# Kernel optimization log

Measured on AMD Instinct MI355X. Metric: run time of the kernel, lower is better.

The kernel has to match this reference:

```python
import jax, jax.numpy as jnp
import numpy as np
from jax import lax

N, C_IN, C_OUT = 1, 16, 32
D = W = H = 48
K = 9                      # num_points (snake kernel size)
CENTER = K // 2
EXTEND_SCOPE = 1.0
EPS = 1e-5
GN_GROUPS = C_OUT // 4
DN = ('NCDHW', 'OIDHW', 'NCDHW')


def conv3d(x, w, strides, padding):
    return lax.conv_general_dilated(x, w, strides, padding, dimension_numbers=DN)


def snake_cumsum(off):
    # off: [N, K, D, W, H]. Cumulative offsets outward from the center point,
    # center forced to 0 (matches the sequential loop in _coordinate_map_3D).
    lower = jnp.flip(jnp.cumsum(jnp.flip(off[:, :CENTER], 1), 1), 1)
    upper = jnp.cumsum(off[:, CENTER + 1:], 1)
    zero = jnp.zeros_like(off[:, :1])
    return jnp.concatenate([lower, zero, upper], axis=1)


def coordinate_map_morph0(off):
    # off: [N, 6K, D, W, H]; morph==0 uses z_offset1 (chans [0,K)) and y_offset1 ([K,2K)).
    cz = snake_cumsum(off[:, :K])
    cy = snake_cumsum(off[:, K:2 * K])
    dt = off.dtype
    zb = jnp.arange(D, dtype=dt)[None, None, :, None, None]
    yb = jnp.arange(W, dtype=dt)[None, None, None, :, None]
    xb = (jnp.arange(H, dtype=dt)[None, None, None, None, :]
          + (jnp.arange(K, dtype=dt) - CENTER)[None, :, None, None, None])
    z = zb + EXTEND_SCOPE * cz                      # [N,K,D,W,H]
    y = yb + EXTEND_SCOPE * cy
    x = jnp.broadcast_to(xb, z.shape)

    def rearr(c):  # [N,K,D,W,H] -> [N,D,W,H*K]  (h-major, k-minor, as in torch permute/reshape)
        return jnp.transpose(c, (0, 2, 3, 4, 1)).reshape(c.shape[0], D, W, H * K)

    return rearr(z), rearr(y), rearr(x)


def trilinear(feat, z, y, x):
    # feat [N,C,D,W,H]; z,y,x [N,D,W,H*K] float coords -> [N,C,D,W,H*K]
    z = jnp.clip(z, 0.0, D - 1.0)
    y = jnp.clip(y, 0.0, W - 1.0)
    x = jnp.clip(x, 0.0, H - 1.0)
    z0 = jnp.clip(jnp.floor(z).astype(jnp.int32), 0, D - 1); z1 = jnp.clip(z0 + 1, 0, D - 1)
    y0 = jnp.clip(jnp.floor(y).astype(jnp.int32), 0, W - 1); y1 = jnp.clip(y0 + 1, 0, W - 1)
    x0 = jnp.clip(jnp.floor(x).astype(jnp.int32), 0, H - 1); x1 = jnp.clip(x0 + 1, 0, H - 1)
    featl = jnp.transpose(feat, (0, 2, 3, 4, 1))  # [N,D,W,H,C]
    b = jnp.arange(feat.shape[0])[:, None, None, None]
    g = lambda zi, yi, xi: featl[b, zi, yi, xi]   # [N,D,W,H*K,C]
    f = feat.dtype
    wz0 = (z1.astype(f) - z)[..., None]; wz1 = (z - z0.astype(f))[..., None]
    wy0 = (y1.astype(f) - y)[..., None]; wy1 = (y - y0.astype(f))[..., None]
    wx0 = (x1.astype(f) - x)[..., None]; wx1 = (x - x0.astype(f))[..., None]
    out = (g(z0, y0, x0) * wz0 * wy0 * wx0 + g(z0, y0, x1) * wz0 * wy0 * wx1
         + g(z0, y1, x0) * wz0 * wy1 * wx0 + g(z0, y1, x1) * wz0 * wy1 * wx1
         + g(z1, y0, x0) * wz1 * wy0 * wx0 + g(z1, y0, x1) * wz1 * wy0 * wx1
         + g(z1, y1, x0) * wz1 * wy1 * wx0 + g(z1, y1, x1) * wz1 * wy1 * wx1)
    return jnp.transpose(out, (0, 4, 1, 2, 3))


def group_norm(x, gamma, beta):
    n = x.shape[0]
    xg = x.reshape(n, GN_GROUPS, -1)
    mu = xg.mean(-1, keepdims=True)
    var = xg.var(-1, keepdims=True)
    xg = (xg - mu) * lax.rsqrt(var + EPS)
    return xg.reshape(x.shape) * gamma[None, :, None, None, None] + beta[None, :, None, None, None]


def setup_inputs() -> dict:
    key = jax.random.key(0)
    ks = jax.random.split(key, 6)
    s = 0.05
    return {
        'x': jax.random.normal(ks[0], (N, C_IN, D, W, H), jnp.float32),
        'ow': jax.random.normal(ks[1], (6 * K, C_IN, 3, 3, 3), jnp.float32) * s,
        'ob': jax.random.normal(ks[2], (6 * K,), jnp.float32) * s,
        'bn_gamma': jnp.ones((6 * K,), jnp.float32),
        'bn_beta': jnp.zeros((6 * K,), jnp.float32),
        'bn_mean': jnp.zeros((6 * K,), jnp.float32),
        'bn_var': jnp.ones((6 * K,), jnp.float32),
        'dw': jax.random.normal(ks[3], (C_OUT, C_IN, 1, 1, K), jnp.float32) * s,
        'db': jax.random.normal(ks[4], (C_OUT,), jnp.float32) * s,
        'gn_gamma': jnp.ones((C_OUT,), jnp.float32),
        'gn_beta': jnp.zeros((C_OUT,), jnp.float32),
    }


def reference(x, ow, ob, bn_gamma, bn_beta, bn_mean, bn_var, dw, db, gn_gamma, gn_beta):
    # offset branch: conv3x3x3 -> BN (eval) -> tanh
    off = conv3d(x, ow, (1, 1, 1), 'SAME') + ob[None, :, None, None, None]
    c = lambda v: v[None, :, None, None, None]
    off = (off - c(bn_mean)) * lax.rsqrt(c(bn_var) + EPS) * c(bn_gamma) + c(bn_beta)
    off = jnp.tanh(off)
    # deformed sampling coordinates (morph 0: spread along x/height axis)
    zc, yc, xc = coordinate_map_morph0(off)
    deformed = trilinear(x, zc, yc, xc)           # [N,C,D,W,H*K]
    # snake conv: kernel (1,1,K) stride (1,1,K) -> [N,C_OUT,D,W,H]
    out = conv3d(deformed, dw, (1, 1, K), 'VALID') + db[None, :, None, None, None]
    out = group_norm(out, gn_gamma, gn_beta)
    return jax.nn.relu(out)
```

## Files before the change

kernel.cpp:

```cpp
#include <hip/hip_runtime.h>

#define DD    48
#define SP    (48*48*48)
#define CIN   16
#define COUT  32
#define KK    9
#define NG    8
#define EPSV  1e-5f

__global__ __launch_bounds__(256) void k_xt(const float* __restrict__ x,
                                            float* __restrict__ xt,
                                            float* __restrict__ stats) {
    int t = threadIdx.x;
    int vb = t >> 2, c = t & 3;
    int v = blockIdx.x * 64 + vb;
    float4 o;
    o.x = x[(4 * c + 0) * SP + v];
    o.y = x[(4 * c + 1) * SP + v];
    o.z = x[(4 * c + 2) * SP + v];
    o.w = x[(4 * c + 3) * SP + v];
    *reinterpret_cast<float4*>(xt + v * 16 + 4 * c) = o;
    if (blockIdx.x == 0) stats[t] = 0.0f;
}

__global__ __launch_bounds__(256) void k_off18(
    const float* __restrict__ xt,  const float* __restrict__ ow,
    const float* __restrict__ ob,  const float* __restrict__ bng,
    const float* __restrict__ bnb, const float* __restrict__ bnm,
    const float* __restrict__ bnv, float* __restrict__ off)
{
    __shared__ float cw[27 * 4 * 72];
    __shared__ float bnsc[18], bnsh[18];

    for (int i = threadIdx.x; i < 27 * CIN * 18; i += 256) {
        int ch = i % 18; int r = i / 18; int ci = r % CIN; int tap = r / CIN;
        int c = ci >> 2, j = ci & 3;
        cw[(tap * 4 + c) * 72 + ch * 4 + j] = ow[(ch * CIN + ci) * 27 + tap];
    }
    if (threadIdx.x < 18) {
        int ch = threadIdx.x;
        float sc = bng[ch] * rsqrtf(bnv[ch] + EPSV);
        bnsc[ch] = sc;
        bnsh[ch] = (ob[ch] - bnm[ch]) * sc + bnb[ch];
    }
    __syncthreads();

    const int nwg = SP / 64;
    int bid = (int)blockIdx.x;
    bid = (bid & 7) * (nwg >> 3) + (bid >> 3);

    const int t  = threadIdx.x;
    const int c  = t & 3;
    const int vb = t >> 2;
    const int v  = bid * 64 + vb;
    const int h = v % DD, w = (v / DD) % DD, d = v / (DD * DD);

    const float* xc = xt + 4 * c;

    float a18[18];
#pragma unroll
    for (int ch = 0; ch < 18; ++ch) a18[ch] = 0.0f;

#pragma unroll
    for (int kd = 0; kd < 3; ++kd) {
        int z = d + kd - 1; bool okz = (unsigned)z < (unsigned)DD;
#pragma unroll
        for (int kw = 0; kw < 3; ++kw) {
            int yy = w + kw - 1; bool oky = (unsigned)yy < (unsigned)DD;
#pragma unroll
            for (int kh = 0; kh < 3; ++kh) {
                int xx = h + kh - 1;
                if (okz && oky && (unsigned)xx < (unsigned)DD) {
                    int tap = (kd * 3 + kw) * 3 + kh;
                    float4 xv = *reinterpret_cast<const float4*>(
                        xc + ((z * DD + yy) * DD + xx) * 16);
                    const float4* wrow = reinterpret_cast<const float4*>(
                        &cw[(tap * 4 + c) * 72]);
#pragma unroll
                    for (int ch = 0; ch < 18; ++ch) {
                        float4 w4 = wrow[ch];
                        a18[ch] += w4.x * xv.x + w4.y * xv.y
                                 + w4.z * xv.z + w4.w * xv.w;
                    }
                }
            }
        }
    }

#pragma unroll
    for (int ch = 0; ch < 18; ++ch) {
        a18[ch] += __shfl_xor(a18[ch], 1);
        a18[ch] += __shfl_xor(a18[ch], 2);
        a18[ch] = tanhf(a18[ch] * bnsc[ch] + bnsh[ch]);
    }

#pragma unroll
    for (int cc = 0; cc < 4; ++cc) {
        if (c == cc) {
#pragma unroll
            for (int j = 0; j < 4; ++j)
                off[(cc * 4 + j) * SP + v] = a18[cc * 4 + j];
        }
    }
    if (c == 0) off[16 * SP + v] = a18[16];
    if (c == 1) off[17 * SP + v] = a18[17];
}

__global__ __launch_bounds__(256) void k_snake(
    const float* __restrict__ xt,  const float* __restrict__ off,
    const float* __restrict__ dw,  const float* __restrict__ db,
    float* __restrict__ pre,       float* __restrict__ stats)
{
    __shared__ float wl[KK * 4 * 132];
    __shared__ float lstat[16];
    for (int i = threadIdx.x; i < KK * CIN * COUT; i += 256) {
        int co = i % COUT; int r = i / COUT; int ci = r % CIN; int k = r / CIN;
        int c = ci >> 2, j = ci & 3;
        wl[(k * 4 + c) * 132 + co * 4 + j] = dw[(co * CIN + ci) * KK + k];
    }
    if (threadIdx.x < 16) lstat[threadIdx.x] = 0.0f;
    __syncthreads();

    const int nwg = SP / 64;
    int bid = (int)blockIdx.x;
    bid = (bid & 7) * (nwg >> 3) + (bid >> 3);

    const int t  = threadIdx.x;
    const int c  = t & 3;
    const int vb = t >> 2;
    const int v  = bid * 64 + vb;
    const int h = v % DD, w = (v / DD) % DD, d = v / (DD * DD);

    float cz[9], cy[9];
    cz[4] = 0.0f; cy[4] = 0.0f;
    {
        float rz = 0.0f, ry = 0.0f;
#pragma unroll
        for (int k = 3; k >= 0; --k) {
            rz += off[k * SP + v];        cz[k] = rz;
            ry += off[(KK + k) * SP + v]; cy[k] = ry;
        }
    }
    {
        float rz = 0.0f, ry = 0.0f;
#pragma unroll
        for (int k = 5; k < KK; ++k) {
            rz += off[k * SP + v];        cz[k] = rz;
            ry += off[(KK + k) * SP + v]; cy[k] = ry;
        }
    }

    float w00[9], w01[9], w10[9], w11[9];
    int   b00[9], b01[9], b10[9], b11[9];
#pragma unroll
    for (int k = 0; k < 9; ++k) {
        int xcol = h + k - 4;
        float m = (xcol >= DD - 1) ? 0.0f : 1.0f;
        if (xcol < 0 || xcol >= DD - 1) xcol = 0;
        float zf = fminf(fmaxf((float)d + cz[k], 0.0f), 47.0f);
        float yf = fminf(fmaxf((float)w + cy[k], 0.0f), 47.0f);
        int z0 = (int)zf, y0 = (int)yf;
        int z1 = min(z0 + 1, 47), y1 = min(y0 + 1, 47);
        float wz1 = zf - (float)z0, wz0 = (float)z1 - zf;
        float wy1 = yf - (float)y0, wy0 = (float)y1 - yf;
        w00[k] = wz0 * wy0 * m; w01[k] = wz0 * wy1 * m;
        w10[k] = wz1 * wy0 * m; w11[k] = wz1 * wy1 * m;
        b00[k] = ((z0 * DD + y0) * DD + xcol) * 16;
        b01[k] = ((z0 * DD + y1) * DD + xcol) * 16;
        b10[k] = ((z1 * DD + y0) * DD + xcol) * 16;
        b11[k] = ((z1 * DD + y1) * DD + xcol) * 16;
    }

    const float* base = xt + 4 * c;
    float acc[COUT];
#pragma unroll
    for (int co = 0; co < COUT; ++co) acc[co] = 0.0f;

    float4 A0, A1, A2, A3, B0, B1, B2, B3;

#define LOADP(P, k)                                                        \
    (P##0) = *reinterpret_cast<const float4*>(base + b00[k]);              \
    (P##1) = *reinterpret_cast<const float4*>(base + b01[k]);              \
    (P##2) = *reinterpret_cast<const float4*>(base + b10[k]);              \
    (P##3) = *reinterpret_cast<const float4*>(base + b11[k]);

#define FMAP(P, k)                                                         \
    {                                                                      \
        float s0 = w00[k]*(P##0).x + w01[k]*(P##1).x + w10[k]*(P##2).x + w11[k]*(P##3).x; \
        float s1 = w00[k]*(P##0).y + w01[k]*(P##1).y + w10[k]*(P##2).y + w11[k]*(P##3).y; \
        float s2 = w00[k]*(P##0).z + w01[k]*(P##1).z + w10[k]*(P##2).z + w11[k]*(P##3).z; \
        float s3 = w00[k]*(P##0).w + w01[k]*(P##1).w + w10[k]*(P##2).w + w11[k]*(P##3).w; \
        const float4* wrow = reinterpret_cast<const float4*>(&wl[((k)*4 + c) * 132]); \
        _Pragma("unroll")                                                  \
        for (int co = 0; co < COUT; ++co) {                                \
            float4 w4 = wrow[co];                                          \
            acc[co] += w4.x * s0 + w4.y * s1 + w4.z * s2 + w4.w * s3;      \
        }                                                                  \
    }

    LOADP(A, 0)
    LOADP(B, 1) FMAP(A, 0)
    LOADP(A, 2) FMAP(B, 1)
    LOADP(B, 3) FMAP(A, 2)
    LOADP(A, 4) FMAP(B, 3)
    LOADP(B, 5) FMAP(A, 4)
    LOADP(A, 6) FMAP(B, 5)
    LOADP(B, 7) FMAP(A, 6)
    LOADP(A, 8) FMAP(B, 7)
    FMAP(A, 8)
#undef LOADP
#undef FMAP

#pragma unroll
    for (int co = 0; co < COUT; ++co) {
        acc[co] += __shfl_xor(acc[co], 1);
        acc[co] += __shfl_xor(acc[co], 2);
        acc[co] += db[co];
    }

#pragma unroll
    for (int cc = 0; cc < 4; ++cc) {
        if (c == cc) {
#pragma unroll
            for (int j = 0; j < 8; ++j)
                pre[(cc * 8 + j) * SP + v] = acc[cc * 8 + j];
        }
    }

#pragma unroll
    for (int g = 0; g < NG; ++g) {
        float a0 = acc[4*g], a1 = acc[4*g+1], a2 = acc[4*g+2], a3 = acc[4*g+3];
        float s  = a0 + a1 + a2 + a3;
        float ss = a0*a0 + a1*a1 + a2*a2 + a3*a3;
#pragma unroll
        for (int o = 4; o <= 32; o <<= 1) {
            s  += __shfl_xor(s,  o);
            ss += __shfl_xor(ss, o);
        }
        if ((t & 63) == 0) {
            atomicAdd(&lstat[g],      s);
            atomicAdd(&lstat[NG + g], ss);
        }
    }
    __syncthreads();
    if (t < 16) atomicAdd(&stats[t * 16], lstat[t]);
}

__global__ __launch_bounds__(256) void k_gn(
    float* __restrict__ buf, const float* __restrict__ stats,
    const float* __restrict__ gamma, const float* __restrict__ beta)
{
    int idx  = blockIdx.x * 256 + threadIdx.x;
    int base = idx * 4;
    int ch = base / SP, g = ch >> 2;

    const float inv_n = 1.0f / (4.0f * (float)SP);
    float mean = stats[g * 16] * inv_n;
    float var  = stats[(NG + g) * 16] * inv_n - mean * mean;
    float rs   = rsqrtf(var + EPSV);
    float ga   = gamma[ch] * rs;
    float be   = beta[ch] - mean * ga;

    float4 p = *reinterpret_cast<const float4*>(buf + base);
    float4 o;
    o.x = fmaxf(p.x * ga + be, 0.0f);
    o.y = fmaxf(p.y * ga + be, 0.0f);
    o.z = fmaxf(p.z * ga + be, 0.0f);
    o.w = fmaxf(p.w * ga + be, 0.0f);
    *reinterpret_cast<float4*>(buf + base) = o;
}

extern "C" void kernel_launch(void* const* d_in, const int* in_sizes, int n_in,
                              void* d_out, int out_size, void* d_ws, size_t ws_size,
                              hipStream_t stream)
{
    const float* x   = (const float*)d_in[0];
    const float* ow  = (const float*)d_in[1];
    const float* ob  = (const float*)d_in[2];
    const float* bng = (const float*)d_in[3];
    const float* bnb = (const float*)d_in[4];
    const float* bnm = (const float*)d_in[5];
    const float* bnv = (const float*)d_in[6];
    const float* dw  = (const float*)d_in[7];
    const float* db  = (const float*)d_in[8];
    const float* gng = (const float*)d_in[9];
    const float* gnb = (const float*)d_in[10];
    float* out = (float*)d_out;

    float* xt    = (float*)d_ws;
    float* stats = xt + CIN * SP;
    float* off   = stats + 256;

    k_xt   <<<SP / 64, 256, 0, stream>>>(x, xt, stats);
    k_off18<<<SP / 64, 256, 0, stream>>>(xt, ow, ob, bng, bnb, bnm, bnv, off);
    k_snake<<<SP / 64, 256, 0, stream>>>(xt, off, dw, db, out, stats);
    k_gn   <<<(COUT * SP / 4) / 256, 256, 0, stream>>>(out, stats, gng, gnb);
}
```

Measured before the change: 223.0 us.

## Compute two adjacent voxels per thread in offset conv and snake kernels

The offset convolution now gives each thread two neighbouring h positions. It loads four input columns per row and reuses them across the three kh taps, and the shared-memory weights are reused for both outputs. The snake kernel also handles two voxels per thread with 128-thread blocks. It interleaves the cumulative offset sum with the tap processing, skips fully masked taps, and uses float2 loads and stores. This roughly doubles per-thread register use and lowers thread count, which may reduce occupancy and latency hiding.

```diff
diff --git a/kernel.cpp b/kernel.cpp
--- a/kernel.cpp
+++ b/kernel.cpp
@@ -45,42 +45,53 @@
     }
     __syncthreads();
 
-    const int nwg = SP / 64;
+    const int nwg = SP / 128;
     int bid = (int)blockIdx.x;
     bid = (bid & 7) * (nwg >> 3) + (bid >> 3);
 
     const int t  = threadIdx.x;
     const int c  = t & 3;
-    const int vb = t >> 2;
-    const int v  = bid * 64 + vb;
-    const int h = v % DD, w = (v / DD) % DD, d = v / (DD * DD);
+    const int vq = t >> 2;
+    const int v0 = bid * 128 + vq * 2;
+    const int h0 = v0 % DD;
+    const int w  = (v0 / DD) % DD;
+    const int d  = v0 / (DD * DD);
 
     const float* xc = xt + 4 * c;
 
-    float a18[18];
-#pragma unroll
-    for (int ch = 0; ch < 18; ++ch) a18[ch] = 0.0f;
+    float a0[18], a1[18];
+#pragma unroll
+    for (int ch = 0; ch < 18; ++ch) { a0[ch] = 0.0f; a1[ch] = 0.0f; }
 
 #pragma unroll
     for (int kd = 0; kd < 3; ++kd) {
         int z = d + kd - 1; bool okz = (unsigned)z < (unsigned)DD;
 #pragma unroll
         for (int kw = 0; kw < 3; ++kw) {
-            int yy = w + kw - 1; bool oky = (unsigned)yy < (unsigned)DD;
-#pragma unroll
-            for (int kh = 0; kh < 3; ++kh) {
-                int xx = h + kh - 1;
-                if (okz && oky && (unsigned)xx < (unsigned)DD) {
+            int yy = w + kw - 1;
+            if (okz && (unsigned)yy < (unsigned)DD) {
+                const float* row = xc + ((z * DD + yy) * DD) * 16;
+                float4 xv[4];
+#pragma unroll
+                for (int j = 0; j < 4; ++j) {
+                    int col = h0 - 1 + j;
+                    float4 val = make_float4(0.f, 0.f, 0.f, 0.f);
+                    if ((unsigned)col < (unsigned)DD)
+                        val = *reinterpret_cast<const float4*>(row + col * 16);
+                    xv[j] = val;
+                }
+#pragma unroll
+                for (int kh = 0; kh < 3; ++kh) {
                     int tap = (kd * 3 + kw) * 3 + kh;
-                    float4 xv = *reinterpret_cast<const float4*>(
-                        xc + ((z * DD + yy) * DD + xx) * 16);
                     const float4* wrow = reinterpret_cast<const float4*>(
                         &cw[(tap * 4 + c) * 72]);
 #pragma unroll
                     for (int ch = 0; ch < 18; ++ch) {
                         float4 w4 = wrow[ch];
-                        a18[ch] += w4.x * xv.x + w4.y * xv.y
-                                 + w4.z * xv.z + w4.w * xv.w;
+                        a0[ch] += w4.x * xv[kh].x + w4.y * xv[kh].y
+                                + w4.z * xv[kh].z + w4.w * xv[kh].w;
+                        a1[ch] += w4.x * xv[kh+1].x + w4.y * xv[kh+1].y
+                                + w4.z * xv[kh+1].z + w4.w * xv[kh+1].w;
                     }
                 }
             }
@@ -89,31 +100,37 @@
 
 #pragma unroll
     for (int ch = 0; ch < 18; ++ch) {
-        a18[ch] += __shfl_xor(a18[ch], 1);
-        a18[ch] += __shfl_xor(a18[ch], 2);
-        a18[ch] = tanhf(a18[ch] * bnsc[ch] + bnsh[ch]);
+        a0[ch] += __shfl_xor(a0[ch], 1);
+        a0[ch] += __shfl_xor(a0[ch], 2);
+        a0[ch] = tanhf(a0[ch] * bnsc[ch] + bnsh[ch]);
+        a1[ch] += __shfl_xor(a1[ch], 1);
+        a1[ch] += __shfl_xor(a1[ch], 2);
+        a1[ch] = tanhf(a1[ch] * bnsc[ch] + bnsh[ch]);
     }
 
 #pragma unroll
     for (int cc = 0; cc < 4; ++cc) {
         if (c == cc) {
 #pragma unroll
-            for (int j = 0; j < 4; ++j)
-                off[(cc * 4 + j) * SP + v] = a18[cc * 4 + j];
-        }
-    }
-    if (c == 0) off[16 * SP + v] = a18[16];
-    if (c == 1) off[17 * SP + v] = a18[17];
-}
-
-__global__ __launch_bounds__(256) void k_snake(
+            for (int j = 0; j < 4; ++j) {
+                int ch = cc * 4 + j;
+                *reinterpret_cast<float2*>(&off[ch * SP + v0]) =
+                    make_float2(a0[ch], a1[ch]);
+            }
+        }
+    }
+    if (c == 0) *reinterpret_cast<float2*>(&off[16 * SP + v0]) = make_float2(a0[16], a1[16]);
+    if (c == 1) *reinterpret_cast<float2*>(&off[17 * SP + v0]) = make_float2(a0[17], a1[17]);
+}
+
+__global__ __launch_bounds__(128) void k_snake(
     const float* __restrict__ xt,  const float* __restrict__ off,
     const float* __restrict__ dw,  const float* __restrict__ db,
     float* __restrict__ pre,       float* __restrict__ stats)
 {
     __shared__ float wl[KK * 4 * 132];
     __shared__ float lstat[16];
-    for (int i = threadIdx.x; i < KK * CIN * COUT; i += 256) {
+    for (int i = threadIdx.x; i < KK * CIN * COUT; i += 128) {
         int co = i % COUT; int r = i / COUT; int ci = r % CIN; int k = r / CIN;
         int c = ci >> 2, j = ci & 3;
         wl[(k * 4 + c) * 132 + co * 4 + j] = dw[(co * CIN + ci) * KK + k];
@@ -127,111 +144,121 @@
 
     const int t  = threadIdx.x;
     const int c  = t & 3;
-    const int vb = t >> 2;
-    const int v  = bid * 64 + vb;
-    const int h = v % DD, w = (v / DD) % DD, d = v / (DD * DD);
-
-    float cz[9], cy[9];
-    cz[4] = 0.0f; cy[4] = 0.0f;
-    {
-        float rz = 0.0f, ry = 0.0f;
-#pragma unroll
-        for (int k = 3; k >= 0; --k) {
-            rz += off[k * SP + v];        cz[k] = rz;
-            ry += off[(KK + k) * SP + v]; cy[k] = ry;
-        }
-    }
-    {
-        float rz = 0.0f, ry = 0.0f;
-#pragma unroll
-        for (int k = 5; k < KK; ++k) {
-            rz += off[k * SP + v];        cz[k] = rz;
-            ry += off[(KK + k) * SP + v]; cy[k] = ry;
-        }
-    }
-
-    float w00[9], w01[9], w10[9], w11[9];
-    int   b00[9], b01[9], b10[9], b11[9];
-#pragma unroll
-    for (int k = 0; k < 9; ++k) {
-        int xcol = h + k - 4;
-        float m = (xcol >= DD - 1) ? 0.0f : 1.0f;
-        if (xcol < 0 || xcol >= DD - 1) xcol = 0;
-        float zf = fminf(fmaxf((float)d + cz[k], 0.0f), 47.0f);
-        float yf = fminf(fmaxf((float)w + cy[k], 0.0f), 47.0f);
+    const int vq = t >> 2;
+    const int v0 = bid * 64 + vq * 2;
+    const int h0 = v0 % DD;
+    const int w  = (v0 / DD) % DD;
+    const int d  = v0 / (DD * DD);
+
+    float acc0[COUT], acc1[COUT];
+#pragma unroll
+    for (int co = 0; co < COUT; ++co) { acc0[co] = 0.0f; acc1[co] = 0.0f; }
+
+    const float* base = xt + 4 * c;
+
+    auto tap = [&](int k, float cz0, float cy0, float cz1, float cy1) {
+        int xc0 = h0 + k - 4;
+        if (xc0 >= DD - 1) return;
+        float m1 = (xc0 + 1 >= DD - 1) ? 0.0f : 1.0f;
+        int a0c = max(xc0, 0);
+        int a1c = max(xc0 + 1, 0);
+
+        float zf = fminf(fmaxf((float)d + cz0, 0.0f), 47.0f);
+        float yf = fminf(fmaxf((float)w + cy0, 0.0f), 47.0f);
         int z0 = (int)zf, y0 = (int)yf;
         int z1 = min(z0 + 1, 47), y1 = min(y0 + 1, 47);
         float wz1 = zf - (float)z0, wz0 = (float)z1 - zf;
         float wy1 = yf - (float)y0, wy0 = (float)y1 - yf;
-        w00[k] = wz0 * wy0 * m; w01[k] = wz0 * wy1 * m;
-        w10[k] = wz1 * wy0 * m; w11[k] = wz1 * wy1 * m;
-        b00[k] = ((z0 * DD + y0) * DD + xcol) * 16;
-        b01[k] = ((z0 * DD + y1) * DD + xcol) * 16;
-        b10[k] = ((z1 * DD + y0) * DD + xcol) * 16;
-        b11[k] = ((z1 * DD + y1) * DD + xcol) * 16;
-    }
-
-    const float* base = xt + 4 * c;
-    float acc[COUT];
-#pragma unroll
-    for (int co = 0; co < COUT; ++co) acc[co] = 0.0f;
-
-    float4 A0, A1, A2, A3, B0, B1, B2, B3;
-
-#define LOADP(P, k)                                                        \
-    (P##0) = *reinterpret_cast<const float4*>(base + b00[k]);              \
-    (P##1) = *reinterpret_cast<const float4*>(base + b01[k]);              \
-    (P##2) = *reinterpret_cast<const float4*>(base + b10[k]);              \
-    (P##3) = *reinterpret_cast<const float4*>(base + b11[k]);
-
-#define FMAP(P, k)                                                         \
-    {                                                                      \
-        float s0 = w00[k]*(P##0).x + w01[k]*(P##1).x + w10[k]*(P##2).x + w11[k]*(P##3).x; \
-        float s1 = w00[k]*(P##0).y + w01[k]*(P##1).y + w10[k]*(P##2).y + w11[k]*(P##3).y; \
-        float s2 = w00[k]*(P##0).z + w01[k]*(P##1).z + w10[k]*(P##2).z + w11[k]*(P##3).z; \
-        float s3 = w00[k]*(P##0).w + w01[k]*(P##1).w + w10[k]*(P##2).w + w11[k]*(P##3).w; \
-        const float4* wrow = reinterpret_cast<const float4*>(&wl[((k)*4 + c) * 132]); \
-        _Pragma("unroll")                                                  \
-        for (int co = 0; co < COUT; ++co) {                                \
-            float4 w4 = wrow[co];                                          \
-            acc[co] += w4.x * s0 + w4.y * s1 + w4.z * s2 + w4.w * s3;      \
-        }                                                                  \
-    }
-
-    LOADP(A, 0)
-    LOADP(B, 1) FMAP(A, 0)
-    LOADP(A, 2) FMAP(B, 1)
-    LOADP(B, 3) FMAP(A, 2)
-    LOADP(A, 4) FMAP(B, 3)
-    LOADP(B, 5) FMAP(A, 4)
-    LOADP(A, 6) FMAP(B, 5)
-    LOADP(B, 7) FMAP(A, 6)
-    LOADP(A, 8) FMAP(B, 7)
-    FMAP(A, 8)
-#undef LOADP
-#undef FMAP
+        float p00 = wz0 * wy0, p01 = wz0 * wy1, p10 = wz1 * wy0, p11 = wz1 * wy1;
+
+        float zg = fminf(fmaxf((float)d + cz1, 0.0f), 47.0f);
+        float yg = fminf(fmaxf((float)w + cy1, 0.0f), 47.0f);
+        int u0 = (int)zg, q0 = (int)yg;
+        int u1 = min(u0 + 1, 47), q1 = min(q0 + 1, 47);
+        float vz1 = zg - (float)u0, vz0 = (float)u1 - zg;
+        float vy1 = yg - (float)q0, vy0 = (float)q1 - yg;
+        float r00 = vz0 * vy0 * m1, r01 = vz0 * vy1 * m1;
+        float r10 = vz1 * vy0 * m1, r11 = vz1 * vy1 * m1;
+
+        float4 A = *reinterpret_cast<const float4*>(base + ((z0 * DD + y0) * DD + a0c) * 16);
+        float4 B = *reinterpret_cast<const float4*>(base + ((z0 * DD + y1) * DD + a0c) * 16);
+        float4 C = *reinterpret_cast<const float4*>(base + ((z1 * DD + y0) * DD + a0c) * 16);
+        float4 E = *reinterpret_cast<const float4*>(base + ((z1 * DD + y1) * DD + a0c) * 16);
+        float s00 = p00 * A.x + p01 * B.x + p10 * C.x + p11 * E.x;
+        float s01 = p00 * A.y + p01 * B.y + p10 * C.y + p11 * E.y;
+        float s02 = p00 * A.z + p01 * B.z + p10 * C.z + p11 * E.z;
+        float s03 = p00 * A.w + p01 * B.w + p10 * C.w + p11 * E.w;
+
+        float4 F = *reinterpret_cast<const float4*>(base + ((u0 * DD + q0) * DD + a1c) * 16);
+        float4 G = *reinterpret_cast<const float4*>(base + ((u0 * DD + q1) * DD + a1c) * 16);
+        float4 H = *reinterpret_cast<const float4*>(base + ((u1 * DD + q0) * DD + a1c) * 16);
+        float4 I = *reinterpret_cast<const float4*>(base + ((u1 * DD + q1) * DD + a1c) * 16);
+        float s10 = r00 * F.x + r01 * G.x + r10 * H.x + r11 * I.x;
+        float s11 = r00 * F.y + r01 * G.y + r10 * H.y + r11 * I.y;
+        float s12 = r00 * F.z + r01 * G.z + r10 * H.z + r11 * I.z;
+        float s13 = r00 * F.w + r01 * G.w + r10 * H.w + r11 * I.w;
+
+        const float4* wrow = reinterpret_cast<const float4*>(&wl[(k * 4 + c) * 132]);
+#pragma unroll
+        for (int co = 0; co < COUT; ++co) {
+            float4 w4 = wrow[co];
+            acc0[co] += w4.x * s00 + w4.y * s01 + w4.z * s02 + w4.w * s03;
+            acc1[co] += w4.x * s10 + w4.y * s11 + w4.z * s12 + w4.w * s13;
+        }
+    };
+
+    tap(4, 0.0f, 0.0f, 0.0f, 0.0f);
+    {
+        float rz0 = 0.0f, ry0 = 0.0f, rz1 = 0.0f, ry1 = 0.0f;
+#pragma unroll
+        for (int k = 3; k >= 0; --k) {
+            float2 oz = *reinterpret_cast<const float2*>(&off[k * SP + v0]);
+            float2 oy = *reinterpret_cast<const float2*>(&off[(KK + k) * SP + v0]);
+            rz0 += oz.x; rz1 += oz.y; ry0 += oy.x; ry1 += oy.y;
+            tap(k, rz0, ry0, rz1, ry1);
+        }
+    }
+    {
+        float rz0 = 0.0f, ry0 = 0.0f, rz1 = 0.0f, ry1 = 0.0f;
+#pragma unroll
+        for (int k = 5; k < KK; ++k) {
+            float2 oz = *reinterpret_cast<const float2*>(&off[k * SP + v0]);
+            float2 oy = *reinterpret_cast<const float2*>(&off[(KK + k) * SP + v0]);
+            rz0 += oz.x; rz1 += oz.y; ry0 += oy.x; ry1 += oy.y;
+            tap(k, rz0, ry0, rz1, ry1);
+        }
+    }
 
 #pragma unroll
     for (int co = 0; co < COUT; ++co) {
-        acc[co] += __shfl_xor(acc[co], 1);
-        acc[co] += __shfl_xor(acc[co], 2);
-        acc[co] += db[co];
+        acc0[co] += __shfl_xor(acc0[co], 1);
+        acc0[co] += __shfl_xor(acc0[co], 2);
+        acc0[co] += db[co];
+        acc1[co] += __shfl_xor(acc1[co], 1);
+        acc1[co] += __shfl_xor(acc1[co], 2);
+        acc1[co] += db[co];
     }
 
 #pragma unroll
     for (int cc = 0; cc < 4; ++cc) {
         if (c == cc) {
 #pragma unroll
-            for (int j = 0; j < 8; ++j)
-                pre[(cc * 8 + j) * SP + v] = acc[cc * 8 + j];
+            for (int j = 0; j < 8; ++j) {
+                int co = cc * 8 + j;
+                *reinterpret_cast<float2*>(&pre[co * SP + v0]) =
+                    make_float2(acc0[co], acc1[co]);
+            }
         }
     }
 
 #pragma unroll
     for (int g = 0; g < NG; ++g) {
-        float a0 = acc[4*g], a1 = acc[4*g+1], a2 = acc[4*g+2], a3 = acc[4*g+3];
-        float s  = a0 + a1 + a2 + a3;
-        float ss = a0*a0 + a1*a1 + a2*a2 + a3*a3;
+        float s  = acc0[4*g] + acc0[4*g+1] + acc0[4*g+2] + acc0[4*g+3]
+                 + acc1[4*g] + acc1[4*g+1] + acc1[4*g+2] + acc1[4*g+3];
+        float ss = acc0[4*g]*acc0[4*g] + acc0[4*g+1]*acc0[4*g+1]
+                 + acc0[4*g+2]*acc0[4*g+2] + acc0[4*g+3]*acc0[4*g+3]
+                 + acc1[4*g]*acc1[4*g] + acc1[4*g+1]*acc1[4*g+1]
+                 + acc1[4*g+2]*acc1[4*g+2] + acc1[4*g+3]*acc1[4*g+3];
 #pragma unroll
         for (int o = 4; o <= 32; o <<= 1) {
             s  += __shfl_xor(s,  o);
@@ -292,7 +319,7 @@
     float* off   = stats + 256;
 
     k_xt   <<<SP / 64, 256, 0, stream>>>(x, xt, stats);
-    k_off18<<<SP / 64, 256, 0, stream>>>(xt, ow, ob, bng, bnb, bnm, bnv, off);
-    k_snake<<<SP / 64, 256, 0, stream>>>(xt, off, dw, db, out, stats);
+    k_off18<<<SP / 128, 256, 0, stream>>>(xt, ow, ob, bng, bnb, bnm, bnv, off);
+    k_snake<<<SP / 64, 128, 0, stream>>>(xt, off, dw, db, out, stats);
     k_gn   <<<(COUT * SP / 4) / 256, 256, 0, stream>>>(out, stats, gng, gnb);
 }
```

After: 260.7 us. 16.9% more time.
